# Kernel tuning notes

Hardware: AMD Instinct MI355X
Metric: run time of the kernel (lower is better)

## Reference

```python
import jax, jax.numpy as jnp
import numpy as np

N_NODES = 100000
N_EDGES = 3200000
D = 16
L = 3


def setup_inputs() -> dict:
    key = jax.random.key(0)
    ks = jax.random.split(key, 7)
    scale = 1.0 / np.sqrt(D)
    x = jax.random.normal(ks[0], (N_NODES, D), dtype=jnp.float32)
    edge_index = jax.random.randint(ks[1], (2, N_EDGES), 0, N_NODES, dtype=jnp.int64)
    Wl = jax.random.normal(ks[2], (L, D, D), dtype=jnp.float32) * scale
    bl = jax.random.normal(ks[3], (L, D), dtype=jnp.float32) * scale
    Wr = jax.random.normal(ks[4], (L, D, D), dtype=jnp.float32) * scale
    Wlin = jax.random.normal(ks[5], (L, D, D), dtype=jnp.float32) * scale
    blin = jax.random.normal(ks[6], (L, D), dtype=jnp.float32) * scale
    return {"x": x, "edge_index": edge_index, "Wl": Wl, "bl": bl,
            "Wr": Wr, "Wlin": Wlin, "blin": blin}


def reference(x, edge_index, Wl, bl, Wr, Wlin, blin):
    src = edge_index[0]
    dst = edge_index[1]
    n = x.shape[0]
    # in-degree for mean aggregation (PyG SAGEConv aggr='mean')
    deg = jax.ops.segment_sum(jnp.ones((src.shape[0],), dtype=x.dtype), dst,
                              num_segments=n)
    denom = jnp.maximum(deg, 1.0)[:, None]  # nodes with no in-edges -> 0 agg
    for i in range(Wl.shape[0]):
        # gather source features, scatter-mean onto targets
        agg = jax.ops.segment_sum(x[src], dst, num_segments=n) / denom
        conv = agg @ Wl[i].T + bl[i] + x @ Wr[i].T  # SAGEConv: lin_l(agg)+lin_r(x)
        x = conv + x @ Wlin[i].T + blin[i]          # + Linear residual
    return x
```

## Files before the change

kernel.cpp:

```cpp
#include <hip/hip_runtime.h>

#define N_NODES 100000
#define N_EDGES 3200000
#define D 16

#define TILE 128
#define NB ((N_NODES + TILE - 1) / TILE)
#define CAP 4608
#define NBLK 500
#define SEG (N_EDGES / NBLK)
#define BINT 1024
#define CVTB 391
#define LT 512
#define N4 (N_NODES * D / 4)

__device__ __forceinline__ unsigned packbf(float a, float b) {
    unsigned ua = __float_as_uint(a); ua += 0x7FFFu + ((ua >> 16) & 1u);
    unsigned ub = __float_as_uint(b); ub += 0x7FFFu + ((ub >> 16) & 1u);
    return (ua >> 16) | (ub & 0xFFFF0000u);
}
#define BLO(u) __uint_as_float((u) << 16)
#define BHI(u) __uint_as_float((u) & 0xFFFF0000u)

__global__ __launch_bounds__(BINT, 8) void pre_kernel(
        const float* __restrict__ x, unsigned* __restrict__ xbf,
        const int* __restrict__ src, const int* __restrict__ dst,
        int* __restrict__ cursor, unsigned* __restrict__ ebuf) {
    __shared__ int lcnt[NB];
    __shared__ int ldiff[NB];
    __shared__ unsigned sorted[SEG];
    __shared__ unsigned short sbkt[SEG];
    __shared__ int wsum[16];
    int tid = threadIdx.x;

    if (blockIdx.x >= NBLK) {
        int t = (blockIdx.x - NBLK) * BINT + tid;
        if (t < N4) {
            float4 v = *(const float4*)(x + (size_t)t * 4);
            uint2 o; o.x = packbf(v.x, v.y); o.y = packbf(v.z, v.w);
            *(uint2*)(xbf + (size_t)t * 2) = o;
        }
        return;
    }

    for (int i = tid; i < NB; i += BINT) lcnt[i] = 0;
    __syncthreads();
    int b0 = blockIdx.x * SEG;
    for (int e = b0 + tid * 4; e < b0 + SEG; e += BINT * 4) {
        int4 d4 = *(const int4*)(dst + e);
        atomicAdd(&lcnt[d4.x >> 7], 1);
        atomicAdd(&lcnt[d4.y >> 7], 1);
        atomicAdd(&lcnt[d4.z >> 7], 1);
        atomicAdd(&lcnt[d4.w >> 7], 1);
    }
    __syncthreads();
    {
        int lane = tid & 63, wv = tid >> 6;
        int v = (tid < NB) ? lcnt[tid] : 0;
        int s = v;
        #pragma unroll
        for (int d_ = 1; d_ < 64; d_ <<= 1) {
            int u = __shfl_up(s, d_, 64);
            if (lane >= d_) s += u;
        }
        if (lane == 63) wsum[wv] = s;
        __syncthreads();
        if (tid == 0) {
            int a = 0;
            #pragma unroll
            for (int i = 0; i < 16; i++) { int t_ = wsum[i]; wsum[i] = a; a += t_; }
        }
        __syncthreads();
        int excl = wsum[wv] + s - v;
        if (tid < NB) {
            int g = v ? (tid * CAP + atomicAdd(&cursor[tid], v)) : 0;
            ldiff[tid] = g - excl;
            lcnt[tid] = excl;
        }
        __syncthreads();
    }
    for (int e = b0 + tid * 4; e < b0 + SEG; e += BINT * 4) {
        int4 d4 = *(const int4*)(dst + e);
        int4 s4 = *(const int4*)(src + e);
        int b_, pos;
        b_ = d4.x >> 7; pos = atomicAdd(&lcnt[b_], 1);
        sorted[pos] = ((unsigned)(d4.x & 127) << 17) | (unsigned)s4.x; sbkt[pos] = (unsigned short)b_;
        b_ = d4.y >> 7; pos = atomicAdd(&lcnt[b_], 1);
        sorted[pos] = ((unsigned)(d4.y & 127) << 17) | (unsigned)s4.y; sbkt[pos] = (unsigned short)b_;
        b_ = d4.z >> 7; pos = atomicAdd(&lcnt[b_], 1);
        sorted[pos] = ((unsigned)(d4.z & 127) << 17) | (unsigned)s4.z; sbkt[pos] = (unsigned short)b_;
        b_ = d4.w >> 7; pos = atomicAdd(&lcnt[b_], 1);
        sorted[pos] = ((unsigned)(d4.w & 127) << 17) | (unsigned)s4.w; sbkt[pos] = (unsigned short)b_;
    }
    __syncthreads();
    for (int i = tid; i < SEG; i += BINT) {
        int b_ = sbkt[i];
        ebuf[ldiff[b_] + i] = sorted[i];
    }
}

#define LDG(j) (*(const uint4*)(xbf + (size_t)(se2[(j) + lane2] & 0x1FFFF) * 8 + ho))
#define ACC8(g) do { \
    acc[0] += BLO((g).x); acc[1] += BHI((g).x); acc[2] += BLO((g).y); acc[3] += BHI((g).y); \
    acc[4] += BLO((g).z); acc[5] += BHI((g).z); acc[6] += BLO((g).w); acc[7] += BHI((g).w); } while (0)

__device__ __forceinline__ void agg_xform(
    const float* __restrict__ xin, const unsigned* __restrict__ xbf,
    const unsigned* se2, const int* lofs, int n_loc,
    const float* sWl, const float* sWc, const float* sbc,
    float* __restrict__ xout, unsigned* __restrict__ xbf_out,
    int emit_bf, int b, int N, int tid) {
    int q = tid & 3;
    int n = b * TILE + n_loc;
    if (n >= N) return;

    float4 xq = *(const float4*)(xin + (size_t)n * D + q * 4);
    float xv[4] = { xq.x, xq.y, xq.z, xq.w };

    int s0 = lofs[n_loc];
    int s1 = lofs[n_loc + 1];
    int deg = s1 - s0;
    int lane2 = q >> 1;
    int ho = (q & 1) * 4;

    float acc[8] = {0.f,0.f,0.f,0.f,0.f,0.f,0.f,0.f};
    int end8 = s0 + (deg & ~7);
    int i = s0;
    if (i < end8) {
        uint4 c0 = LDG(i + 0), c1 = LDG(i + 2), c2 = LDG(i + 4), c3 = LDG(i + 6);
        i += 8;
        for (; i < end8; i += 8) {
            uint4 n0 = LDG(i + 0), n1 = LDG(i + 2), n2 = LDG(i + 4), n3 = LDG(i + 6);
            ACC8(c0); ACC8(c1); ACC8(c2); ACC8(c3);
            c0 = n0; c1 = n1; c2 = n2; c3 = n3;
        }
        ACC8(c0); ACC8(c1); ACC8(c2); ACC8(c3);
    }
    for (; i + 2 <= s1; i += 2) {
        uint4 g = LDG(i);
        ACC8(g);
    }
    if (i < s1 && lane2 == 0) {
        uint4 g = *(const uint4*)(xbf + (size_t)(se2[i] & 0x1FFFF) * 8 + ho);
        ACC8(g);
    }
    #pragma unroll
    for (int k = 0; k < 8; k++) acc[k] += __shfl_xor(acc[k], 2, 4);

    int srcAbs = (tid & 63 & ~3) | (q >> 1);
    float inv = 1.0f / fmaxf((float)deg, 1.0f);
    float a[4];
    #pragma unroll
    for (int k = 0; k < 4; k++) {
        float lo = __shfl(acc[k], srcAbs);
        float hi = __shfl(acc[4 + k], srcAbs);
        a[k] = ((q & 1) ? hi : lo) * inv;
    }

    float o[4];
    #pragma unroll
    for (int j = 0; j < D; j++) {
        float p = 0.f;
        #pragma unroll
        for (int k = 0; k < 4; k++) {
            int kk = q * 4 + k;
            p += a[k] * sWl[j * D + kk] + xv[k] * sWc[j * D + kk];
        }
        p += __shfl_xor(p, 1, 4);
        p += __shfl_xor(p, 2, 4);
        if ((j >> 2) == q) o[j & 3] = p + sbc[j];
    }
    *(float4*)(xout + (size_t)n * D + q * 4) = make_float4(o[0], o[1], o[2], o[3]);
    if (emit_bf) {
        uint2 ob; ob.x = packbf(o[0], o[1]); ob.y = packbf(o[2], o[3]);
        *(uint2*)(xbf_out + (size_t)n * 8 + q * 2) = ob;
    }
}

__global__ void layer0_kernel(
        const float* __restrict__ xin, const unsigned* __restrict__ xbf,
        unsigned* __restrict__ ebuf, const int* __restrict__ cnt,
        int* __restrict__ node_start, int* __restrict__ gperm,
        const float* __restrict__ Wl, const float* __restrict__ bl,
        const float* __restrict__ Wr, const float* __restrict__ Wlin,
        const float* __restrict__ blin,
        float* __restrict__ xout, unsigned* __restrict__ xbf_out, int N) {
    __shared__ unsigned se[CAP];
    __shared__ unsigned se2[CAP];
    __shared__ int lcnt[TILE];
    __shared__ int lofs[TILE + 1];
    __shared__ int sdeg[TILE];
    __shared__ int perm[TILE];
    __shared__ float sWl[D * D];
    __shared__ float sWc[D * D];
    __shared__ float sbc[D];

    int tid = threadIdx.x;
    int b = blockIdx.x;
    int base = b * CAP;
    int nE = min(cnt[b], CAP);
    int nE4 = (nE + 3) >> 2;

    if (tid < D * D) { sWl[tid] = Wl[tid]; sWc[tid] = Wr[tid] + Wlin[tid]; }
    if (tid < D) sbc[tid] = bl[tid] + blin[tid];
    if (tid < TILE) lcnt[tid] = 0;
    for (int i = tid; i < nE4; i += LT)
        ((uint4*)se)[i] = ((const uint4*)(ebuf + base))[i];
    __syncthreads();
    for (int i = tid; i < nE; i += LT)
        atomicAdd(&lcnt[se[i] >> 17], 1);
    __syncthreads();
    if (tid < 64) {
        int l2 = tid * 2;
        int c0 = lcnt[l2], c1 = lcnt[l2 + 1];
        int v = c0 + c1, s = v;
        #pragma unroll
        for (int d_ = 1; d_ < 64; d_ <<= 1) {
            int u = __shfl_up(s, d_, 64);
            if (tid >= d_) s += u;
        }
        int excl = s - v;
        lofs[l2] = excl; sdeg[l2] = c0; lcnt[l2] = excl;
        node_start[b * TILE + l2] = excl;
        int e1 = excl + c0;
        lofs[l2 + 1] = e1; sdeg[l2 + 1] = c1; lcnt[l2 + 1] = e1;
        node_start[b * TILE + l2 + 1] = e1;
        if (tid == 63) lofs[TILE] = s;
    }
    __syncthreads();
    if (tid < TILE) {
        int dm = sdeg[tid];
        int r = 0;
        for (int j = 0; j < TILE; j++) {
            int dj = sdeg[j];
            r += (dj > dm) || (dj == dm && j < tid);
        }
        perm[r] = tid;
        gperm[b * TILE + r] = tid;
    }
    for (int i = tid; i < nE; i += LT) {
        unsigned p = se[i];
        int pos = atomicAdd(&lcnt[p >> 17], 1);
        se2[pos] = p;
    }
    __syncthreads();
    for (int i = tid; i < nE4; i += LT)
        ((uint4*)(ebuf + base))[i] = ((const uint4*)se2)[i];

    agg_xform(xin, xbf, se2, lofs, perm[tid >> 2], sWl, sWc, sbc,
              xout, xbf_out, 1, b, N, tid);
}

__global__ __launch_bounds__(LT, 8) void layerN_kernel(
        const float* __restrict__ xin, const unsigned* __restrict__ xbf,
        const unsigned* __restrict__ ebuf, const int* __restrict__ cnt,
        const int* __restrict__ node_start, const int* __restrict__ gperm,
        const float* __restrict__ Wl, const float* __restrict__ bl,
        const float* __restrict__ Wr, const float* __restrict__ Wlin,
        const float* __restrict__ blin,
        float* __restrict__ xout, unsigned* __restrict__ xbf_out,
        int emit_bf, int N) {
    __shared__ unsigned se2[CAP];
    __shared__ int lofs[TILE + 1];
    __shared__ float sWl[D * D];
    __shared__ float sWc[D * D];
    __shared__ float sbc[D];

    int tid = threadIdx.x;
    int b = blockIdx.x;
    int base = b * CAP;
    int nE = min(cnt[b], CAP);
    int nE4 = (nE + 3) >> 2;

    if (tid < D * D) { sWl[tid] = Wl[tid]; sWc[tid] = Wr[tid] + Wlin[tid]; }
    if (tid < D) sbc[tid] = bl[tid] + blin[tid];
    if (tid < TILE) lofs[tid] = node_start[b * TILE + tid];
    if (tid == 0) lofs[TILE] = nE;
    for (int i = tid; i < nE4; i += LT)
        ((uint4*)se2)[i] = ((const uint4*)(ebuf + base))[i];
    int n_loc = gperm[b * TILE + (tid >> 2)];
    __syncthreads();

    agg_xform(xin, xbf, se2, lofs, n_loc, sWl, sWc, sbc,
              xout, xbf_out, emit_bf, b, N, tid);
}

extern "C" void kernel_launch(void* const* d_in, const int* in_sizes, int n_in,
                              void* d_out, int out_size, void* d_ws, size_t ws_size,
                              hipStream_t stream) {
    const float* x    = (const float*)d_in[0];
    const int*   ei   = (const int*)d_in[1];
    const float* Wl   = (const float*)d_in[2];
    const float* bl   = (const float*)d_in[3];
    const float* Wr   = (const float*)d_in[4];
    const float* Wlin = (const float*)d_in[5];
    const float* blin = (const float*)d_in[6];
    float* out = (float*)d_out;

    const int* src = ei;
    const int* dst = ei + N_EDGES;

    char* w = (char*)d_ws;
    unsigned* ebuf   = (unsigned*)w;  w += (size_t)NB * CAP * 4;
    float* bufA      = (float*)w;     w += (size_t)N_NODES * D * 4;
    float* bufB      = (float*)w;     w += (size_t)N_NODES * D * 4;
    unsigned* xbf0   = (unsigned*)w;  w += (size_t)N_NODES * 8 * 4;
    unsigned* xbf1   = (unsigned*)w;  w += (size_t)N_NODES * 8 * 4;
    int*   cursor    = (int*)w;       w += (size_t)NB * 4;
    int*   node_start= (int*)w;       w += (size_t)NB * TILE * 4;
    int*   gperm     = (int*)w;       w += (size_t)NB * TILE * 4;

    hipMemsetAsync(cursor, 0, (size_t)NB * 4, stream);
    pre_kernel<<<NBLK + CVTB, BINT, 0, stream>>>(x, xbf0, src, dst, cursor, ebuf);

    layer0_kernel<<<NB, LT, 0, stream>>>(
        x, xbf0, ebuf, cursor, node_start, gperm,
        Wl, bl, Wr, Wlin, blin, bufA, xbf1, N_NODES);
    layerN_kernel<<<NB, LT, 0, stream>>>(
        bufA, xbf1, ebuf, cursor, node_start, gperm,
        Wl + D * D, bl + D, Wr + D * D, Wlin + D * D, blin + D, bufB, xbf0, 1, N_NODES);
    layerN_kernel<<<NB, LT, 0, stream>>>(
        bufB, xbf0, ebuf, cursor, node_start, gperm,
        Wl + 2 * D * D, bl + 2 * D, Wr + 2 * D * D, Wlin + 2 * D * D, blin + 2 * D,
        out, nullptr, 0, N_NODES);
}
```

Before: 193.6 us.

## Fuse preprocessing and all three layers into one cooperative persistent kernel

Replaces the pre-pass kernel and the three per-layer kernels with one cooperative kernel of NB/2 blocks. Grid-wide syncs separate the edge bucketing from the three layers. Each block keeps the sorted edge lists and permutations for its two tiles in shared memory across all layers, so the per-layer reload and re-sort from the bucket buffer goes away, along with kernel launch gaps. The risks are lower parallelism (fewer blocks, each doing two tiles serially), grid-sync overhead, and the shared-memory size limiting occupancy. If cooperative launch is unavailable, it falls back to the old multi-kernel path.

```diff
diff --git a/kernel.cpp b/kernel.cpp
--- a/kernel.cpp
+++ b/kernel.cpp
@@ -1,4 +1,7 @@
 #include <hip/hip_runtime.h>
+#include <hip/hip_cooperative_groups.h>
+
+namespace cg = cooperative_groups;
 
 #define N_NODES 100000
 #define N_EDGES 3200000
@@ -7,12 +10,15 @@
 #define TILE 128
 #define NB ((N_NODES + TILE - 1) / TILE)
 #define CAP 4608
+#define LT 512
+#define GRID (NB / 2)
+#define SEGR 4096
+#define N4 (N_NODES * D / 4)
+
 #define NBLK 500
 #define SEG (N_EDGES / NBLK)
 #define BINT 1024
 #define CVTB 391
-#define LT 512
-#define N4 (N_NODES * D / 4)
 
 __device__ __forceinline__ unsigned packbf(float a, float b) {
     unsigned ua = __float_as_uint(a); ua += 0x7FFFu + ((ua >> 16) & 1u);
@@ -21,6 +27,265 @@
 }
 #define BLO(u) __uint_as_float((u) << 16)
 #define BHI(u) __uint_as_float((u) & 0xFFFF0000u)
+
+#define LDG(j) (*(const uint4*)(xbf + (size_t)(se2[(j) + lane2] & 0x1FFFF) * 8 + ho))
+#define ACC8(g) do { \
+    acc[0] += BLO((g).x); acc[1] += BHI((g).x); acc[2] += BLO((g).y); acc[3] += BHI((g).y); \
+    acc[4] += BLO((g).z); acc[5] += BHI((g).z); acc[6] += BLO((g).w); acc[7] += BHI((g).w); } while (0)
+
+__device__ __forceinline__ void agg_xform(
+    const float* __restrict__ xin, const unsigned* __restrict__ xbf,
+    const unsigned* se2, const int* lofs, int n_loc,
+    const float* sWl, const float* sWc, const float* sbc,
+    float* __restrict__ xout, unsigned* __restrict__ xbf_out,
+    int emit_bf, int b, int N, int tid) {
+    int q = tid & 3;
+    int n = b * TILE + n_loc;
+    if (n < N) {
+        float4 xq = *(const float4*)(xin + (size_t)n * D + q * 4);
+        float xv[4] = { xq.x, xq.y, xq.z, xq.w };
+
+        int s0 = lofs[n_loc];
+        int s1 = lofs[n_loc + 1];
+        int deg = s1 - s0;
+        int lane2 = q >> 1;
+        int ho = (q & 1) * 4;
+
+        float acc[8] = {0.f,0.f,0.f,0.f,0.f,0.f,0.f,0.f};
+        int end8 = s0 + (deg & ~7);
+        int i = s0;
+        if (i < end8) {
+            uint4 c0 = LDG(i + 0), c1 = LDG(i + 2), c2 = LDG(i + 4), c3 = LDG(i + 6);
+            i += 8;
+            for (; i < end8; i += 8) {
+                uint4 n0 = LDG(i + 0), n1 = LDG(i + 2), n2 = LDG(i + 4), n3 = LDG(i + 6);
+                ACC8(c0); ACC8(c1); ACC8(c2); ACC8(c3);
+                c0 = n0; c1 = n1; c2 = n2; c3 = n3;
+            }
+            ACC8(c0); ACC8(c1); ACC8(c2); ACC8(c3);
+        }
+        for (; i + 2 <= s1; i += 2) {
+            uint4 g = LDG(i);
+            ACC8(g);
+        }
+        if (i < s1 && lane2 == 0) {
+            uint4 g = *(const uint4*)(xbf + (size_t)(se2[i] & 0x1FFFF) * 8 + ho);
+            ACC8(g);
+        }
+        #pragma unroll
+        for (int k = 0; k < 8; k++) acc[k] += __shfl_xor(acc[k], 2, 4);
+
+        int srcAbs = (tid & 63 & ~3) | (q >> 1);
+        float inv = 1.0f / fmaxf((float)deg, 1.0f);
+        float a[4];
+        #pragma unroll
+        for (int k = 0; k < 4; k++) {
+            float lo = __shfl(acc[k], srcAbs);
+            float hi = __shfl(acc[4 + k], srcAbs);
+            a[k] = ((q & 1) ? hi : lo) * inv;
+        }
+
+        float o[4];
+        #pragma unroll
+        for (int j = 0; j < D; j++) {
+            float p = 0.f;
+            #pragma unroll
+            for (int k = 0; k < 4; k++) {
+                int kk = q * 4 + k;
+                p += a[k] * sWl[j * D + kk] + xv[k] * sWc[j * D + kk];
+            }
+            p += __shfl_xor(p, 1, 4);
+            p += __shfl_xor(p, 2, 4);
+            if ((j >> 2) == q) o[j & 3] = p + sbc[j];
+        }
+        *(float4*)(xout + (size_t)n * D + q * 4) = make_float4(o[0], o[1], o[2], o[3]);
+        if (emit_bf) {
+            uint2 ob; ob.x = packbf(o[0], o[1]); ob.y = packbf(o[2], o[3]);
+            *(uint2*)(xbf_out + (size_t)n * 8 + q * 2) = ob;
+        }
+    }
+}
+
+struct SmemA {
+    int lcnt[NB];
+    int ldiff[NB];
+    unsigned sorted[SEGR];
+    unsigned short sbkt[SEGR];
+    int wsum[8];
+};
+struct SmemB {
+    unsigned se2[2][CAP];
+    int lofs[2][TILE + 1];
+    int perm[2][TILE];
+    int lc[TILE];
+    int sdeg[TILE];
+    float sWl[D * D];
+    float sWc[D * D];
+    float sbc[D];
+};
+union Smem { SmemA a; SmemB b; };
+
+__global__ __launch_bounds__(LT, 4) void fused_kernel(
+        const float* __restrict__ x, const int* __restrict__ src, const int* __restrict__ dst,
+        const float* __restrict__ Wl, const float* __restrict__ bl,
+        const float* __restrict__ Wr, const float* __restrict__ Wlin,
+        const float* __restrict__ blin,
+        float* __restrict__ out, unsigned* __restrict__ ebuf,
+        float* __restrict__ bufA, float* __restrict__ bufB,
+        unsigned* __restrict__ xbf0, unsigned* __restrict__ xbf1,
+        int* __restrict__ cursor) {
+    __shared__ Smem sm;
+    cg::grid_group grid = cg::this_grid();
+    int tid = threadIdx.x;
+    int b = blockIdx.x;
+
+    for (int t = b * LT + tid; t < N4; t += GRID * LT) {
+        float4 v = *(const float4*)(x + (size_t)t * 4);
+        uint2 o; o.x = packbf(v.x, v.y); o.y = packbf(v.z, v.w);
+        *(uint2*)(xbf0 + (size_t)t * 2) = o;
+    }
+
+    for (int r = 0; r < 2; ++r) {
+        int e0 = b * (2 * SEGR) + r * SEGR;
+        int eEnd = min(e0 + SEGR, N_EDGES);
+        int nSeg = eEnd - e0;
+        __syncthreads();
+        for (int i = tid; i < NB; i += LT) sm.a.lcnt[i] = 0;
+        __syncthreads();
+        for (int e = e0 + tid * 4; e < eEnd; e += LT * 4) {
+            int4 d4 = *(const int4*)(dst + e);
+            atomicAdd(&sm.a.lcnt[d4.x >> 7], 1);
+            atomicAdd(&sm.a.lcnt[d4.y >> 7], 1);
+            atomicAdd(&sm.a.lcnt[d4.z >> 7], 1);
+            atomicAdd(&sm.a.lcnt[d4.w >> 7], 1);
+        }
+        __syncthreads();
+        {
+            int lane = tid & 63, wv = tid >> 6;
+            int i2 = tid * 2;
+            int c0 = (i2 < NB) ? sm.a.lcnt[i2] : 0;
+            int c1 = (i2 + 1 < NB) ? sm.a.lcnt[i2 + 1] : 0;
+            int v = c0 + c1, s = v;
+            #pragma unroll
+            for (int d_ = 1; d_ < 64; d_ <<= 1) {
+                int u = __shfl_up(s, d_, 64);
+                if (lane >= d_) s += u;
+            }
+            if (lane == 63) sm.a.wsum[wv] = s;
+            __syncthreads();
+            if (tid == 0) {
+                int a_ = 0;
+                for (int i = 0; i < 8; i++) { int t_ = sm.a.wsum[i]; sm.a.wsum[i] = a_; a_ += t_; }
+            }
+            __syncthreads();
+            int excl = sm.a.wsum[wv] + s - v;
+            if (i2 < NB) {
+                int g = c0 ? (i2 * CAP + atomicAdd(&cursor[i2], c0)) : 0;
+                sm.a.ldiff[i2] = g - excl;
+                sm.a.lcnt[i2] = excl;
+            }
+            if (i2 + 1 < NB) {
+                int e1 = excl + c0;
+                int g = c1 ? ((i2 + 1) * CAP + atomicAdd(&cursor[i2 + 1], c1)) : 0;
+                sm.a.ldiff[i2 + 1] = g - e1;
+                sm.a.lcnt[i2 + 1] = e1;
+            }
+            __syncthreads();
+        }
+        for (int e = e0 + tid * 4; e < eEnd; e += LT * 4) {
+            int4 d4 = *(const int4*)(dst + e);
+            int4 s4 = *(const int4*)(src + e);
+            int b_, pos;
+            b_ = d4.x >> 7; pos = atomicAdd(&sm.a.lcnt[b_], 1);
+            sm.a.sorted[pos] = ((unsigned)(d4.x & 127) << 17) | (unsigned)s4.x; sm.a.sbkt[pos] = (unsigned short)b_;
+            b_ = d4.y >> 7; pos = atomicAdd(&sm.a.lcnt[b_], 1);
+            sm.a.sorted[pos] = ((unsigned)(d4.y & 127) << 17) | (unsigned)s4.y; sm.a.sbkt[pos] = (unsigned short)b_;
+            b_ = d4.z >> 7; pos = atomicAdd(&sm.a.lcnt[b_], 1);
+            sm.a.sorted[pos] = ((unsigned)(d4.z & 127) << 17) | (unsigned)s4.z; sm.a.sbkt[pos] = (unsigned short)b_;
+            b_ = d4.w >> 7; pos = atomicAdd(&sm.a.lcnt[b_], 1);
+            sm.a.sorted[pos] = ((unsigned)(d4.w & 127) << 17) | (unsigned)s4.w; sm.a.sbkt[pos] = (unsigned short)b_;
+        }
+        __syncthreads();
+        for (int i = tid; i < nSeg; i += LT)
+            ebuf[sm.a.ldiff[sm.a.sbkt[i]] + i] = sm.a.sorted[i];
+    }
+
+    __threadfence();
+    grid.sync();
+
+    for (int bk = 0; bk < 2; ++bk) {
+        int B = 2 * b + bk;
+        int base = B * CAP;
+        int nE = min(cursor[B], CAP);
+        int nE4 = (nE + 3) >> 2;
+        __syncthreads();
+        if (tid < TILE) sm.b.lc[tid] = 0;
+        __syncthreads();
+        for (int i4 = tid; i4 < nE4; i4 += LT) {
+            uint4 qv = ((const uint4*)(ebuf + base))[i4];
+            int k0 = i4 * 4;
+            if (k0 < nE)     atomicAdd(&sm.b.lc[qv.x >> 17], 1);
+            if (k0 + 1 < nE) atomicAdd(&sm.b.lc[qv.y >> 17], 1);
+            if (k0 + 2 < nE) atomicAdd(&sm.b.lc[qv.z >> 17], 1);
+            if (k0 + 3 < nE) atomicAdd(&sm.b.lc[qv.w >> 17], 1);
+        }
+        __syncthreads();
+        if (tid < 64) {
+            int l2 = tid * 2;
+            int c0 = sm.b.lc[l2], c1 = sm.b.lc[l2 + 1];
+            int v = c0 + c1, s = v;
+            #pragma unroll
+            for (int d_ = 1; d_ < 64; d_ <<= 1) {
+                int u = __shfl_up(s, d_, 64);
+                if (tid >= d_) s += u;
+            }
+            int excl = s - v;
+            sm.b.lofs[bk][l2] = excl; sm.b.sdeg[l2] = c0; sm.b.lc[l2] = excl;
+            int e1 = excl + c0;
+            sm.b.lofs[bk][l2 + 1] = e1; sm.b.sdeg[l2 + 1] = c1; sm.b.lc[l2 + 1] = e1;
+            if (tid == 63) sm.b.lofs[bk][TILE] = s;
+        }
+        __syncthreads();
+        if (tid < TILE) {
+            int dm = sm.b.sdeg[tid];
+            int rk = 0;
+            for (int j = 0; j < TILE; j++) {
+                int dj = sm.b.sdeg[j];
+                rk += (dj > dm) || (dj == dm && j < tid);
+            }
+            sm.b.perm[bk][rk] = tid;
+        }
+        for (int i4 = tid; i4 < nE4; i4 += LT) {
+            uint4 qv = ((const uint4*)(ebuf + base))[i4];
+            int k0 = i4 * 4;
+            if (k0 < nE)     { int pos = atomicAdd(&sm.b.lc[qv.x >> 17], 1); sm.b.se2[bk][pos] = qv.x; }
+            if (k0 + 1 < nE) { int pos = atomicAdd(&sm.b.lc[qv.y >> 17], 1); sm.b.se2[bk][pos] = qv.y; }
+            if (k0 + 2 < nE) { int pos = atomicAdd(&sm.b.lc[qv.z >> 17], 1); sm.b.se2[bk][pos] = qv.z; }
+            if (k0 + 3 < nE) { int pos = atomicAdd(&sm.b.lc[qv.w >> 17], 1); sm.b.se2[bk][pos] = qv.w; }
+        }
+    }
+    __syncthreads();
+
+    for (int l = 0; l < 3; ++l) {
+        if (l) { __threadfence(); grid.sync(); }
+        if (tid < D * D) {
+            sm.b.sWl[tid] = Wl[l * D * D + tid];
+            sm.b.sWc[tid] = Wr[l * D * D + tid] + Wlin[l * D * D + tid];
+        }
+        if (tid < D) sm.b.sbc[tid] = bl[l * D + tid] + blin[l * D + tid];
+        __syncthreads();
+        const float* xin = (l == 0) ? x : (l == 1) ? bufA : bufB;
+        float* xout = (l == 0) ? bufA : (l == 1) ? bufB : out;
+        const unsigned* xbin = (l == 1) ? xbf1 : xbf0;
+        unsigned* xbout = (l == 1) ? xbf0 : xbf1;
+        for (int bk = 0; bk < 2; ++bk) {
+            int B = 2 * b + bk;
+            agg_xform(xin, xbin, sm.b.se2[bk], sm.b.lofs[bk], sm.b.perm[bk][tid >> 2],
+                      sm.b.sWl, sm.b.sWc, sm.b.sbc,
+                      xout, xbout, (l < 2) ? 1 : 0, B, N_NODES, tid);
+        }
+    }
+}
 
 __global__ __launch_bounds__(BINT, 8) void pre_kernel(
         const float* __restrict__ x, unsigned* __restrict__ xbf,
@@ -96,84 +361,6 @@
     for (int i = tid; i < SEG; i += BINT) {
         int b_ = sbkt[i];
         ebuf[ldiff[b_] + i] = sorted[i];
-    }
-}
-
-#define LDG(j) (*(const uint4*)(xbf + (size_t)(se2[(j) + lane2] & 0x1FFFF) * 8 + ho))
-#define ACC8(g) do { \
-    acc[0] += BLO((g).x); acc[1] += BHI((g).x); acc[2] += BLO((g).y); acc[3] += BHI((g).y); \
-    acc[4] += BLO((g).z); acc[5] += BHI((g).z); acc[6] += BLO((g).w); acc[7] += BHI((g).w); } while (0)
-
-__device__ __forceinline__ void agg_xform(
-    const float* __restrict__ xin, const unsigned* __restrict__ xbf,
-    const unsigned* se2, const int* lofs, int n_loc,
-    const float* sWl, const float* sWc, const float* sbc,
-    float* __restrict__ xout, unsigned* __restrict__ xbf_out,
-    int emit_bf, int b, int N, int tid) {
-    int q = tid & 3;
-    int n = b * TILE + n_loc;
-    if (n >= N) return;
-
-    float4 xq = *(const float4*)(xin + (size_t)n * D + q * 4);
-    float xv[4] = { xq.x, xq.y, xq.z, xq.w };
-
-    int s0 = lofs[n_loc];
-    int s1 = lofs[n_loc + 1];
-    int deg = s1 - s0;
-    int lane2 = q >> 1;
-    int ho = (q & 1) * 4;
-
-    float acc[8] = {0.f,0.f,0.f,0.f,0.f,0.f,0.f,0.f};
-    int end8 = s0 + (deg & ~7);
-    int i = s0;
-    if (i < end8) {
-        uint4 c0 = LDG(i + 0), c1 = LDG(i + 2), c2 = LDG(i + 4), c3 = LDG(i + 6);
-        i += 8;
-        for (; i < end8; i += 8) {
-            uint4 n0 = LDG(i + 0), n1 = LDG(i + 2), n2 = LDG(i + 4), n3 = LDG(i + 6);
-            ACC8(c0); ACC8(c1); ACC8(c2); ACC8(c3);
-            c0 = n0; c1 = n1; c2 = n2; c3 = n3;
-        }
-        ACC8(c0); ACC8(c1); ACC8(c2); ACC8(c3);
-    }
-    for (; i + 2 <= s1; i += 2) {
-        uint4 g = LDG(i);
-        ACC8(g);
-    }
-    if (i < s1 && lane2 == 0) {
-        uint4 g = *(const uint4*)(xbf + (size_t)(se2[i] & 0x1FFFF) * 8 + ho);
-        ACC8(g);
-    }
-    #pragma unroll
-    for (int k = 0; k < 8; k++) acc[k] += __shfl_xor(acc[k], 2, 4);
-
-    int srcAbs = (tid & 63 & ~3) | (q >> 1);
-    float inv = 1.0f / fmaxf((float)deg, 1.0f);
-    float a[4];
-    #pragma unroll
-    for (int k = 0; k < 4; k++) {
-        float lo = __shfl(acc[k], srcAbs);
-        float hi = __shfl(acc[4 + k], srcAbs);
-        a[k] = ((q & 1) ? hi : lo) * inv;
-    }
-
-    float o[4];
-    #pragma unroll
-    for (int j = 0; j < D; j++) {
-        float p = 0.f;
-        #pragma unroll
-        for (int k = 0; k < 4; k++) {
-            int kk = q * 4 + k;
-            p += a[k] * sWl[j * D + kk] + xv[k] * sWc[j * D + kk];
-        }
-        p += __shfl_xor(p, 1, 4);
-        p += __shfl_xor(p, 2, 4);
-        if ((j >> 2) == q) o[j & 3] = p + sbc[j];
-    }
-    *(float4*)(xout + (size_t)n * D + q * 4) = make_float4(o[0], o[1], o[2], o[3]);
-    if (emit_bf) {
-        uint2 ob; ob.x = packbf(o[0], o[1]); ob.y = packbf(o[2], o[3]);
-        *(uint2*)(xbf_out + (size_t)n * 8 + q * 2) = ob;
     }
 }
 
@@ -306,21 +493,44 @@
     float* bufB      = (float*)w;     w += (size_t)N_NODES * D * 4;
     unsigned* xbf0   = (unsigned*)w;  w += (size_t)N_NODES * 8 * 4;
     unsigned* xbf1   = (unsigned*)w;  w += (size_t)N_NODES * 8 * 4;
-    int*   cursor    = (int*)w;       w += (size_t)NB * 4;
-    int*   node_start= (int*)w;       w += (size_t)NB * TILE * 4;
-    int*   gperm     = (int*)w;       w += (size_t)NB * TILE * 4;
+    int* cursor      = (int*)w;       w += (size_t)NB * 4;
+    int* node_start  = (int*)w;       w += (size_t)NB * TILE * 4;
+    int* gperm       = (int*)w;       w += (size_t)NB * TILE * 4;
+
+    static int coop_ok = -1;
+    if (coop_ok < 0) {
+        int dev = 0;
+        hipGetDevice(&dev);
+        int coop_attr = 0, numCU = 0, maxb = 0;
+        hipDeviceGetAttribute(&coop_attr, hipDeviceAttributeCooperativeLaunch, dev);
+        hipDeviceGetAttribute(&numCU, hipDeviceAttributeMultiprocessorCount, dev);
+        hipError_t oe = hipOccupancyMaxActiveBlocksPerMultiprocessor(
+            &maxb, (const void*)fused_kernel, LT, 0);
+        coop_ok = (coop_attr && oe == hipSuccess && maxb > 0 &&
+                   (long)maxb * (long)numCU >= (long)GRID) ? 1 : 0;
+    }
 
     hipMemsetAsync(cursor, 0, (size_t)NB * 4, stream);
-    pre_kernel<<<NBLK + CVTB, BINT, 0, stream>>>(x, xbf0, src, dst, cursor, ebuf);
-
-    layer0_kernel<<<NB, LT, 0, stream>>>(
-        x, xbf0, ebuf, cursor, node_start, gperm,
-        Wl, bl, Wr, Wlin, blin, bufA, xbf1, N_NODES);
-    layerN_kernel<<<NB, LT, 0, stream>>>(
-        bufA, xbf1, ebuf, cursor, node_start, gperm,
-        Wl + D * D, bl + D, Wr + D * D, Wlin + D * D, blin + D, bufB, xbf0, 1, N_NODES);
-    layerN_kernel<<<NB, LT, 0, stream>>>(
-        bufB, xbf0, ebuf, cursor, node_start, gperm,
-        Wl + 2 * D * D, bl + 2 * D, Wr + 2 * D * D, Wlin + 2 * D * D, blin + 2 * D,
-        out, nullptr, 0, N_NODES);
-}
+
+    if (coop_ok) {
+        void* args[] = { (void*)&x, (void*)&src, (void*)&dst, (void*)&Wl, (void*)&bl,
+                         (void*)&Wr, (void*)&Wlin, (void*)&blin, (void*)&out, (void*)&ebuf,
+                         (void*)&bufA, (void*)&bufB, (void*)&xbf0, (void*)&xbf1, (void*)&cursor };
+        hipError_t le = hipLaunchCooperativeKernel((const void*)fused_kernel,
+                                                   dim3(GRID), dim3(LT), args, 0, stream);
+        if (le != hipSuccess) coop_ok = 0;
+    }
+    if (!coop_ok) {
+        pre_kernel<<<NBLK + CVTB, BINT, 0, stream>>>(x, xbf0, src, dst, cursor, ebuf);
+        layer0_kernel<<<NB, LT, 0, stream>>>(
+            x, xbf0, ebuf, cursor, node_start, gperm,
+            Wl, bl, Wr, Wlin, blin, bufA, xbf1, N_NODES);
+        layerN_kernel<<<NB, LT, 0, stream>>>(
+            bufA, xbf1, ebuf, cursor, node_start, gperm,
+            Wl + D * D, bl + D, Wr + D * D, Wlin + D * D, blin + D, bufB, xbf0, 1, N_NODES);
+        layerN_kernel<<<NB, LT, 0, stream>>>(
+            bufB, xbf0, ebuf, cursor, node_start, gperm,
+            Wl + 2 * D * D, bl + 2 * D, Wr + 2 * D * D, Wlin + 2 * D * D, blin + 2 * D,
+            out, nullptr, 0, N_NODES);
+    }
+}
```

After: 194.8 us. No clear change (+0.6%).

## Switch aggregation to edge-balanced segmented reduction with shared-memory atomics

Applied to the files above, without the earlier changes.

Replaces per-node gather loops, which relied on a degree-sorted permutation, with an edge-parallel scheme. Each pair of threads takes an equal contiguous chunk of the destination-sorted edge list, accumulates runs that share a destination, and flushes partial sums into a shared-memory accumulator with atomics. A separate pass then applies the dense transform per node. This removes load imbalance from varying degrees and the permutation computation, at the cost of an extra shared buffer, shared atomics, a barrier, and lower occupancy bounds.

```diff
diff --git a/kernel.cpp b/kernel.cpp
--- a/kernel.cpp
+++ b/kernel.cpp
@@ -99,63 +99,73 @@
     }
 }
 
-#define LDG(j) (*(const uint4*)(xbf + (size_t)(se2[(j) + lane2] & 0x1FFFF) * 8 + ho))
 #define ACC8(g) do { \
     acc[0] += BLO((g).x); acc[1] += BHI((g).x); acc[2] += BLO((g).y); acc[3] += BHI((g).y); \
     acc[4] += BLO((g).z); acc[5] += BHI((g).z); acc[6] += BLO((g).w); acc[7] += BHI((g).w); } while (0)
 
-__device__ __forceinline__ void agg_xform(
-    const float* __restrict__ xin, const unsigned* __restrict__ xbf,
-    const unsigned* se2, const int* lofs, int n_loc,
-    const float* sWl, const float* sWc, const float* sbc,
-    float* __restrict__ xout, unsigned* __restrict__ xbf_out,
-    int emit_bf, int b, int N, int tid) {
+__device__ __forceinline__ void agg_edges(
+        const unsigned* __restrict__ xbf, const unsigned* se2, int nE,
+        float* accf, int tid) {
+    int pr = tid >> 1;
+    int fb = (tid & 1) * 8;
+    int ho = (tid & 1) * 4;
+    int CH = (nE + 255) >> 8;
+    int e0 = pr * CH;
+    int e1 = min(e0 + CH, nE);
+    float acc[8] = {0.f,0.f,0.f,0.f,0.f,0.f,0.f,0.f};
+    int cur = -1;
+    for (int e = e0; e < e1; e += 8) {
+        int em1 = e1 - 1;
+        unsigned pk[8];
+        uint4 g[8];
+        #pragma unroll
+        for (int j = 0; j < 8; j++) {
+            pk[j] = se2[min(e + j, em1)];
+            g[j] = *(const uint4*)(xbf + (size_t)(pk[j] & 0x1FFFF) * 8 + ho);
+        }
+        int lim = e1 - e;
+        #pragma unroll
+        for (int j = 0; j < 8; j++) {
+            if (j < lim) {
+                int nd = (int)(pk[j] >> 17);
+                if (nd != cur) {
+                    if (cur >= 0) {
+                        #pragma unroll
+                        for (int k = 0; k < 8; k++) {
+                            atomicAdd(&accf[cur * 16 + fb + k], acc[k]);
+                            acc[k] = 0.f;
+                        }
+                    }
+                    cur = nd;
+                }
+                ACC8(g[j]);
+            }
+        }
+    }
+    if (cur >= 0) {
+        #pragma unroll
+        for (int k = 0; k < 8; k++)
+            atomicAdd(&accf[cur * 16 + fb + k], acc[k]);
+    }
+}
+
+__device__ __forceinline__ void xform_store(
+        const float* __restrict__ xin, float* __restrict__ xout,
+        unsigned* __restrict__ xbf_out, int emit_bf,
+        const float* accf, const int* lofs,
+        const float* sWl, const float* sWc, const float* sbc,
+        int b, int N, int tid) {
     int q = tid & 3;
+    int n_loc = tid >> 2;
     int n = b * TILE + n_loc;
     if (n >= N) return;
-
+    int deg = lofs[n_loc + 1] - lofs[n_loc];
+    float inv = 1.0f / fmaxf((float)deg, 1.0f);
     float4 xq = *(const float4*)(xin + (size_t)n * D + q * 4);
     float xv[4] = { xq.x, xq.y, xq.z, xq.w };
-
-    int s0 = lofs[n_loc];
-    int s1 = lofs[n_loc + 1];
-    int deg = s1 - s0;
-    int lane2 = q >> 1;
-    int ho = (q & 1) * 4;
-
-    float acc[8] = {0.f,0.f,0.f,0.f,0.f,0.f,0.f,0.f};
-    int end8 = s0 + (deg & ~7);
-    int i = s0;
-    if (i < end8) {
-        uint4 c0 = LDG(i + 0), c1 = LDG(i + 2), c2 = LDG(i + 4), c3 = LDG(i + 6);
-        i += 8;
-        for (; i < end8; i += 8) {
-            uint4 n0 = LDG(i + 0), n1 = LDG(i + 2), n2 = LDG(i + 4), n3 = LDG(i + 6);
-            ACC8(c0); ACC8(c1); ACC8(c2); ACC8(c3);
-            c0 = n0; c1 = n1; c2 = n2; c3 = n3;
-        }
-        ACC8(c0); ACC8(c1); ACC8(c2); ACC8(c3);
-    }
-    for (; i + 2 <= s1; i += 2) {
-        uint4 g = LDG(i);
-        ACC8(g);
-    }
-    if (i < s1 && lane2 == 0) {
-        uint4 g = *(const uint4*)(xbf + (size_t)(se2[i] & 0x1FFFF) * 8 + ho);
-        ACC8(g);
-    }
-    #pragma unroll
-    for (int k = 0; k < 8; k++) acc[k] += __shfl_xor(acc[k], 2, 4);
-
-    int srcAbs = (tid & 63 & ~3) | (q >> 1);
-    float inv = 1.0f / fmaxf((float)deg, 1.0f);
     float a[4];
     #pragma unroll
-    for (int k = 0; k < 4; k++) {
-        float lo = __shfl(acc[k], srcAbs);
-        float hi = __shfl(acc[4 + k], srcAbs);
-        a[k] = ((q & 1) ? hi : lo) * inv;
-    }
+    for (int k = 0; k < 4; k++) a[k] = accf[n_loc * 16 + q * 4 + k] * inv;
 
     float o[4];
     #pragma unroll
@@ -177,10 +187,10 @@
     }
 }
 
-__global__ void layer0_kernel(
+__global__ __launch_bounds__(LT, 6) void layer0_kernel(
         const float* __restrict__ xin, const unsigned* __restrict__ xbf,
         unsigned* __restrict__ ebuf, const int* __restrict__ cnt,
-        int* __restrict__ node_start, int* __restrict__ gperm,
+        int* __restrict__ node_start,
         const float* __restrict__ Wl, const float* __restrict__ bl,
         const float* __restrict__ Wr, const float* __restrict__ Wlin,
         const float* __restrict__ blin,
@@ -189,8 +199,7 @@
     __shared__ unsigned se2[CAP];
     __shared__ int lcnt[TILE];
     __shared__ int lofs[TILE + 1];
-    __shared__ int sdeg[TILE];
-    __shared__ int perm[TILE];
+    __shared__ float accf[TILE * 16];
     __shared__ float sWl[D * D];
     __shared__ float sWc[D * D];
     __shared__ float sbc[D];
@@ -204,6 +213,7 @@
     if (tid < D * D) { sWl[tid] = Wl[tid]; sWc[tid] = Wr[tid] + Wlin[tid]; }
     if (tid < D) sbc[tid] = bl[tid] + blin[tid];
     if (tid < TILE) lcnt[tid] = 0;
+    for (int i = tid; i < TILE * 16; i += LT) accf[i] = 0.f;
     for (int i = tid; i < nE4; i += LT)
         ((uint4*)se)[i] = ((const uint4*)(ebuf + base))[i];
     __syncthreads();
@@ -220,24 +230,14 @@
             if (tid >= d_) s += u;
         }
         int excl = s - v;
-        lofs[l2] = excl; sdeg[l2] = c0; lcnt[l2] = excl;
+        lofs[l2] = excl; lcnt[l2] = excl;
         node_start[b * TILE + l2] = excl;
         int e1 = excl + c0;
-        lofs[l2 + 1] = e1; sdeg[l2 + 1] = c1; lcnt[l2 + 1] = e1;
+        lofs[l2 + 1] = e1; lcnt[l2 + 1] = e1;
         node_start[b * TILE + l2 + 1] = e1;
         if (tid == 63) lofs[TILE] = s;
     }
     __syncthreads();
-    if (tid < TILE) {
-        int dm = sdeg[tid];
-        int r = 0;
-        for (int j = 0; j < TILE; j++) {
-            int dj = sdeg[j];
-            r += (dj > dm) || (dj == dm && j < tid);
-        }
-        perm[r] = tid;
-        gperm[b * TILE + r] = tid;
-    }
     for (int i = tid; i < nE; i += LT) {
         unsigned p = se[i];
         int pos = atomicAdd(&lcnt[p >> 17], 1);
@@ -247,14 +247,15 @@
     for (int i = tid; i < nE4; i += LT)
         ((uint4*)(ebuf + base))[i] = ((const uint4*)se2)[i];
 
-    agg_xform(xin, xbf, se2, lofs, perm[tid >> 2], sWl, sWc, sbc,
-              xout, xbf_out, 1, b, N, tid);
-}
-
-__global__ __launch_bounds__(LT, 8) void layerN_kernel(
+    agg_edges(xbf, se2, nE, accf, tid);
+    __syncthreads();
+    xform_store(xin, xout, xbf_out, 1, accf, lofs, sWl, sWc, sbc, b, N, tid);
+}
+
+__global__ __launch_bounds__(LT, 6) void layerN_kernel(
         const float* __restrict__ xin, const unsigned* __restrict__ xbf,
         const unsigned* __restrict__ ebuf, const int* __restrict__ cnt,
-        const int* __restrict__ node_start, const int* __restrict__ gperm,
+        const int* __restrict__ node_start,
         const float* __restrict__ Wl, const float* __restrict__ bl,
         const float* __restrict__ Wr, const float* __restrict__ Wlin,
         const float* __restrict__ blin,
@@ -262,6 +263,7 @@
         int emit_bf, int N) {
     __shared__ unsigned se2[CAP];
     __shared__ int lofs[TILE + 1];
+    __shared__ float accf[TILE * 16];
     __shared__ float sWl[D * D];
     __shared__ float sWc[D * D];
     __shared__ float sbc[D];
@@ -276,13 +278,14 @@
     if (tid < D) sbc[tid] = bl[tid] + blin[tid];
     if (tid < TILE) lofs[tid] = node_start[b * TILE + tid];
     if (tid == 0) lofs[TILE] = nE;
+    for (int i = tid; i < TILE * 16; i += LT) accf[i] = 0.f;
     for (int i = tid; i < nE4; i += LT)
         ((uint4*)se2)[i] = ((const uint4*)(ebuf + base))[i];
-    int n_loc = gperm[b * TILE + (tid >> 2)];
-    __syncthreads();
-
-    agg_xform(xin, xbf, se2, lofs, n_loc, sWl, sWc, sbc,
-              xout, xbf_out, emit_bf, b, N, tid);
+    __syncthreads();
+
+    agg_edges(xbf, se2, nE, accf, tid);
+    __syncthreads();
+    xform_store(xin, xout, xbf_out, emit_bf, accf, lofs, sWl, sWc, sbc, b, N, tid);
 }
 
 extern "C" void kernel_launch(void* const* d_in, const int* in_sizes, int n_in,
@@ -308,19 +311,18 @@
     unsigned* xbf1   = (unsigned*)w;  w += (size_t)N_NODES * 8 * 4;
     int*   cursor    = (int*)w;       w += (size_t)NB * 4;
     int*   node_start= (int*)w;       w += (size_t)NB * TILE * 4;
-    int*   gperm     = (int*)w;       w += (size_t)NB * TILE * 4;
-
-    hipMemsetAsync(cursor, 0, (size_t)NB * 4, stream);
+
+    (void)hipMemsetAsync(cursor, 0, (size_t)NB * 4, stream);
     pre_kernel<<<NBLK + CVTB, BINT, 0, stream>>>(x, xbf0, src, dst, cursor, ebuf);
 
     layer0_kernel<<<NB, LT, 0, stream>>>(
-        x, xbf0, ebuf, cursor, node_start, gperm,
+        x, xbf0, ebuf, cursor, node_start,
         Wl, bl, Wr, Wlin, blin, bufA, xbf1, N_NODES);
     layerN_kernel<<<NB, LT, 0, stream>>>(
-        bufA, xbf1, ebuf, cursor, node_start, gperm,
+        bufA, xbf1, ebuf, cursor, node_start,
         Wl + D * D, bl + D, Wr + D * D, Wlin + D * D, blin + D, bufB, xbf0, 1, N_NODES);
     layerN_kernel<<<NB, LT, 0, stream>>>(
-        bufB, xbf0, ebuf, cursor, node_start, gperm,
+        bufB, xbf0, ebuf, cursor, node_start,
         Wl + 2 * D * D, bl + 2 * D, Wr + 2 * D * D, Wlin + 2 * D * D, blin + 2 * D,
         out, nullptr, 0, N_NODES);
 }
```

Result: slower. 252.9 us (+30.6%).
